# Kernel tuning notes

Hardware: AMD Instinct MI355X
Metric: run time of the kernel (lower is better)

The kernel has to match this reference:

```python
import jax, jax.numpy as jnp
import numpy as np

B, N, F_IN = 32, 1024, 128
H1, H2, OUT = 64, 32, 10
EDGE_P = 0.01  # edge probability for random adjacency


def setup_inputs() -> dict:
    key = jax.random.key(0)
    ks = jax.random.split(key, 16)
    x = jax.random.normal(ks[0], (B, N, F_IN), dtype=jnp.float32)
    # dense binary adjacency per graph (module consumes dense [N,N] adj)
    adj = (jax.random.uniform(ks[1], (B, N, N)) < EDGE_P).astype(jnp.float32)
    mask = jnp.ones((B, N, 1), dtype=jnp.float32)
    s = 0.05
    W1a = jax.random.normal(ks[2], (F_IN, H1), dtype=jnp.float32) * s
    b1a = jnp.zeros((H1,), dtype=jnp.float32)
    W2a = jax.random.normal(ks[3], (H1, H1), dtype=jnp.float32) * s
    b2a = jnp.zeros((H1,), dtype=jnp.float32)
    W1b = jax.random.normal(ks[4], (H1, H2), dtype=jnp.float32) * s
    b1b = jnp.zeros((H2,), dtype=jnp.float32)
    W2b = jax.random.normal(ks[5], (H2, H2), dtype=jnp.float32) * s
    b2b = jnp.zeros((H2,), dtype=jnp.float32)
    Wfc = jax.random.normal(ks[6], (H2, OUT), dtype=jnp.float32) * s
    bfc = jnp.zeros((OUT,), dtype=jnp.float32)
    return dict(x=x, adj=adj, mask=mask, W1a=W1a, b1a=b1a, W2a=W2a, b2a=b2a,
                W1b=W1b, b1b=b1b, W2b=W2b, b2b=b2b, Wfc=Wfc, bfc=bfc)


def _gin_layer(h, adj, mask, Wa, ba, Wb, bb, eps=0.0):
    # neighbor sum aggregation: neigh[b,i] = sum_j adj[b,i,j] * h[b,j]
    neigh = jnp.einsum('bij,bjf->bif', adj, h)
    z = (1.0 + eps) * h + neigh
    z = jax.nn.relu(z @ Wa + ba) @ Wb + bb  # 2-layer MLP
    return z * mask  # zero out padded nodes


def reference(x, adj, mask, W1a, b1a, W2a, b2a, W1b, b1b, W2b, b2b, Wfc, bfc):
    h = _gin_layer(x, adj, mask, W1a, b1a, W2a, b2a)   # [B,N,64]
    h = _gin_layer(h, adj, mask, W1b, b1b, W2b, b2b)   # [B,N,32]
    g = jnp.max(h, axis=1)                              # graph readout [B,32]
    return g @ Wfc + bfc                                # [B,OUT] (dropout = eval identity)
```

## Files before the change

### kernel.cpp

```cpp
#include <hip/hip_runtime.h>
#include <cstdint>
#include <cstddef>


#define CAP 64

typedef float v4f __attribute__((ext_vector_type(4)));

__device__ __forceinline__ float rl(float x, int l) {
  return __int_as_float(__builtin_amdgcn_readlane(__float_as_int(x), l));
}

__global__ __launch_bounds__(256) void k_scanproj(
    const float* __restrict__ x, const float* __restrict__ W1a,
    float* __restrict__ u,
    const float* __restrict__ adj, int* __restrict__ nbr,
    int* __restrict__ deg) {
  __shared__ float sW[128 * 64];
  int lane = threadIdx.x & 63;
  int wid  = threadIdx.x >> 6;
  if (blockIdx.x < 1024) {
    for (int t = threadIdx.x; t < 128 * 64; t += 256) sW[t] = W1a[t];
    __syncthreads();
    int row0 = (blockIdx.x * 4 + wid) * 8;
    row0 = __builtin_amdgcn_readfirstlane(row0);
    const float* xr = x + (size_t)row0 * 128;
    float acc[8] = {0, 0, 0, 0, 0, 0, 0, 0};
    for (int kc = 0; kc < 32; ++kc) {
      v4f xv[8];
      #pragma unroll
      for (int r = 0; r < 8; ++r)
        xv[r] = *(const v4f*)(xr + r * 128 + kc * 4);
      #pragma unroll
      for (int j = 0; j < 4; ++j) {
        float w = sW[(kc * 4 + j) * 64 + lane];
        #pragma unroll
        for (int r = 0; r < 8; ++r)
          acc[r] = fmaf(xv[r][j], w, acc[r]);
      }
    }
    #pragma unroll
    for (int r = 0; r < 8; ++r)
      u[(size_t)(row0 + r) * 64 + lane] = acc[r];
  } else {
    int node = (blockIdx.x - 1024) * 4 + wid;
    const v4f* arow = (const v4f*)(adj + (size_t)node * 1024);
    int* outp = nbr + node * CAP;
    v4f a[4];
    #pragma unroll
    for (int c = 0; c < 4; ++c)
      a[c] = __builtin_nontemporal_load(arow + c * 64 + lane);
    int cnt = 0;
    #pragma unroll
    for (int c = 0; c < 4; ++c) {
      #pragma unroll
      for (int comp = 0; comp < 4; ++comp) {
        bool hit = (a[c][comp] != 0.0f);
        unsigned long long m = __ballot(hit);
        if (hit) {
          int below = __builtin_amdgcn_mbcnt_hi(
              (unsigned)(m >> 32),
              __builtin_amdgcn_mbcnt_lo((unsigned)m, 0));
          int pos = cnt + below;
          if (pos < CAP) outp[pos] = ((c * 64 + lane) << 2) + comp;
        }
        cnt += __popcll(m);
      }
    }
    if (lane == 0) deg[node] = cnt < CAP ? cnt : CAP;
  }
}

__global__ __launch_bounds__(256) void k_gathA(
    const float* __restrict__ u, const int* __restrict__ nbr,
    const int* __restrict__ deg, const float* __restrict__ mask,
    const float* __restrict__ b1a, const float* __restrict__ W2a,
    const float* __restrict__ b2a, const float* __restrict__ W1b,
    float* __restrict__ v) {
  __shared__ float sW2[64 * 64];
  __shared__ float sW1b[64 * 32];
  for (int t = threadIdx.x; t < 64 * 64; t += 256) sW2[t] = W2a[t];
  for (int t = threadIdx.x; t < 64 * 32; t += 256) sW1b[t] = W1b[t];
  __syncthreads();
  int lane = threadIdx.x & 63;
  int f = lane & 31, hh = lane >> 5;
  float ba1 = b1a[lane], ba2 = b2a[lane];
  int gw = blockIdx.x * 4 + (threadIdx.x >> 6);
  int n0 = gw * 2, n1 = n0 + 1;
  const float* ub = u + (size_t)(n0 & ~1023) * 64;
  int d0 = deg[n0], d1 = deg[n1];
  int nl0 = nbr[n0 * CAP + lane], nl1 = nbr[n1 * CAP + lane];
  float s0[8] = {0,0,0,0,0,0,0,0}, s1[8] = {0,0,0,0,0,0,0,0};
  int dmax = d0 > d1 ? d0 : d1;
  int rounds = (dmax + 7) >> 3;
  for (int rr = 0; rr < rounds; ++rr) {
    int base = rr << 3;
    #pragma unroll
    for (int i = 0; i < 8; ++i) {
      int t = base + i;
      int j0 = __builtin_amdgcn_readlane(nl0, t);
      int j1 = __builtin_amdgcn_readlane(nl1, t);
      bool ok0 = t < d0, ok1 = t < d1;
      j0 = ok0 ? j0 : 0;  j1 = ok1 ? j1 : 0;
      float v0 = ub[j0 * 64 + lane];
      float v1 = ub[j1 * 64 + lane];
      s0[i] += ok0 ? v0 : 0.0f;
      s1[i] += ok1 ? v1 : 0.0f;
    }
  }
  float acc0 = ub[(n0 & 1023) * 64 + lane]
             + (((s0[0]+s0[1])+(s0[2]+s0[3]))+((s0[4]+s0[5])+(s0[6]+s0[7])));
  float acc1 = ub[(n1 & 1023) * 64 + lane]
             + (((s1[0]+s1[1])+(s1[2]+s1[3]))+((s1[4]+s1[5])+(s1[6]+s1[7])));
  float r0 = fmaxf(acc0 + ba1, 0.0f);
  float r1 = fmaxf(acc1 + ba1, 0.0f);
  float a0=0,a1=0,a2=0,a3=0, c0=0,c1=0,c2=0,c3=0;
  #pragma unroll
  for (int k = 0; k < 64; k += 4) {
    float w0 = sW2[(k    ) * 64 + lane];
    float w1 = sW2[(k + 1) * 64 + lane];
    float w2 = sW2[(k + 2) * 64 + lane];
    float w3 = sW2[(k + 3) * 64 + lane];
    a0 = fmaf(rl(r0, k    ), w0, a0);  c0 = fmaf(rl(r1, k    ), w0, c0);
    a1 = fmaf(rl(r0, k + 1), w1, a1);  c1 = fmaf(rl(r1, k + 1), w1, c1);
    a2 = fmaf(rl(r0, k + 2), w2, a2);  c2 = fmaf(rl(r1, k + 2), w2, c2);
    a3 = fmaf(rl(r0, k + 3), w3, a3);  c3 = fmaf(rl(r1, k + 3), w3, c3);
  }
  float h20 = (ba2 + ((a0 + a1) + (a2 + a3))) * mask[n0];
  float h21 = (ba2 + ((c0 + c1) + (c2 + c3))) * mask[n1];
  float p00=0,p01=0, p10=0,p11=0;
  #pragma unroll
  for (int k0 = 0; k0 < 32; k0 += 2) {
    float w0 = sW1b[(hh * 32 + k0    ) * 32 + f];
    float w1 = sW1b[(hh * 32 + k0 + 1) * 32 + f];
    p00 = fmaf(__shfl(h20, hh * 32 + k0    ), w0, p00);
    p01 = fmaf(__shfl(h20, hh * 32 + k0 + 1), w1, p01);
    p10 = fmaf(__shfl(h21, hh * 32 + k0    ), w0, p10);
    p11 = fmaf(__shfl(h21, hh * 32 + k0 + 1), w1, p11);
  }
  float vp0 = p00 + p01;  vp0 += __shfl_xor(vp0, 32);
  float vp1 = p10 + p11;  vp1 += __shfl_xor(vp1, 32);
  if (hh == 0) {
    v[n0 * 32 + f] = vp0;
    v[n1 * 32 + f] = vp1;
  }
}

__global__ __launch_bounds__(256) void k_gathB(
    const float* __restrict__ v, const int* __restrict__ nbr,
    const int* __restrict__ deg, const float* __restrict__ mask,
    const float* __restrict__ b1b, const float* __restrict__ W2b,
    const float* __restrict__ b2b, float* __restrict__ h3) {
  __shared__ float sW2b[32 * 32];
  for (int t = threadIdx.x; t < 32 * 32; t += 256) sW2b[t] = W2b[t];
  __syncthreads();
  int lane = threadIdx.x & 63;
  int f = lane & 31, hh = lane >> 5;
  float bb1 = b1b[f], bb2 = b2b[f];
  int gw = blockIdx.x * 4 + (threadIdx.x >> 6);
  int n0 = gw * 2, n1 = n0 + 1;
  const float* vb = v + (size_t)(n0 & ~1023) * 32;
  int d0 = deg[n0], d1 = deg[n1];
  int nl0 = nbr[n0 * CAP + lane], nl1 = nbr[n1 * CAP + lane];
  float s0[8] = {0,0,0,0,0,0,0,0}, s1[8] = {0,0,0,0,0,0,0,0};
  int dmax = d0 > d1 ? d0 : d1;
  int rounds = (dmax + 15) >> 4;
  for (int rr = 0; rr < rounds; ++rr) {
    int base = rr << 4;
    #pragma unroll
    for (int i = 0; i < 8; ++i) {
      int t = base + (i << 1) + hh;
      int j0 = __shfl(nl0, t);
      int j1 = __shfl(nl1, t);
      bool ok0 = t < d0, ok1 = t < d1;
      j0 = ok0 ? j0 : 0;  j1 = ok1 ? j1 : 0;
      float v0 = vb[j0 * 32 + f];
      float v1 = vb[j1 * 32 + f];
      s0[i] += ok0 ? v0 : 0.0f;
      s1[i] += ok1 ? v1 : 0.0f;
    }
  }
  float acc0 = ((s0[0]+s0[1])+(s0[2]+s0[3]))+((s0[4]+s0[5])+(s0[6]+s0[7]));
  float acc1 = ((s1[0]+s1[1])+(s1[2]+s1[3]))+((s1[4]+s1[5])+(s1[6]+s1[7]));
  acc0 += __shfl_xor(acc0, 32);
  acc1 += __shfl_xor(acc1, 32);
  float r0 = fmaxf(vb[(n0 & 1023) * 32 + f] + acc0 + bb1, 0.0f);
  float r1 = fmaxf(vb[(n1 & 1023) * 32 + f] + acc1 + bb1, 0.0f);
  float a0=0,a1=0,a2=0,a3=0, c0=0,c1=0,c2=0,c3=0;
  #pragma unroll
  for (int k = 0; k < 32; k += 4) {
    float w0 = sW2b[(k    ) * 32 + f];
    float w1 = sW2b[(k + 1) * 32 + f];
    float w2 = sW2b[(k + 2) * 32 + f];
    float w3 = sW2b[(k + 3) * 32 + f];
    a0 = fmaf(rl(r0, k    ), w0, a0);  c0 = fmaf(rl(r1, k    ), w0, c0);
    a1 = fmaf(rl(r0, k + 1), w1, a1);  c1 = fmaf(rl(r1, k + 1), w1, c1);
    a2 = fmaf(rl(r0, k + 2), w2, a2);  c2 = fmaf(rl(r1, k + 2), w2, c2);
    a3 = fmaf(rl(r0, k + 3), w3, a3);  c3 = fmaf(rl(r1, k + 3), w3, c3);
  }
  float o0 = (bb2 + ((a0 + a1) + (a2 + a3))) * mask[n0];
  float o1 = (bb2 + ((c0 + c1) + (c2 + c3))) * mask[n1];
  if (hh == 0) {
    h3[n0 * 32 + f] = o0;
    h3[n1 * 32 + f] = o1;
  }
}

__global__ __launch_bounds__(1024) void k_readout(
    const float* __restrict__ h3, const float* __restrict__ Wfc,
    const float* __restrict__ bfc, float* __restrict__ out) {
  __shared__ float red[32][33];
  __shared__ float g[32];
  int b = blockIdx.x;
  int f = threadIdx.x & 31, c = threadIdx.x >> 5;
  const float* hb = h3 + (size_t)b * 1024 * 32;
  float m = -3.4e38f;
  for (int r0 = 0; r0 < 32; ++r0)
    m = fmaxf(m, hb[(c * 32 + r0) * 32 + f]);
  red[c][f] = m;
  __syncthreads();
  if (c == 0) {
    float mm = red[0][f];
    #pragma unroll
    for (int k = 1; k < 32; ++k) mm = fmaxf(mm, red[k][f]);
    g[f] = mm;
  }
  __syncthreads();
  if (threadIdx.x < 10) {
    float o = bfc[threadIdx.x];
    #pragma unroll
    for (int k = 0; k < 32; ++k)
      o = fmaf(g[k], Wfc[k * 10 + threadIdx.x], o);
    out[b * 10 + threadIdx.x] = o;
  }
}

extern "C" void kernel_launch(void* const* d_in, const int* in_sizes, int n_in,
                              void* d_out, int out_size, void* d_ws, size_t ws_size,
                              hipStream_t stream) {
  const float* x    = (const float*)d_in[0];
  const float* adj  = (const float*)d_in[1];
  const float* mask = (const float*)d_in[2];
  const float* W1a  = (const float*)d_in[3];
  const float* b1a  = (const float*)d_in[4];
  const float* W2a  = (const float*)d_in[5];
  const float* b2a  = (const float*)d_in[6];
  const float* W1b  = (const float*)d_in[7];
  const float* b1b  = (const float*)d_in[8];
  const float* W2b  = (const float*)d_in[9];
  const float* b2b  = (const float*)d_in[10];
  const float* Wfc  = (const float*)d_in[11];
  const float* bfc  = (const float*)d_in[12];
  float* out = (float*)d_out;

  char* ws = (char*)d_ws;
  float* u   = (float*)(ws);
  float* v   = (float*)(ws + (8u << 20));
  int*   nbr = (int*)  (ws + (12u << 20));
  int*   deg = (int*)  (ws + (20u << 20));
  float* h3  = (float*)(ws);

  hipLaunchKernelGGL(k_scanproj, dim3(9216), dim3(256),  0, stream,
                     x, W1a, u, adj, nbr, deg);
  hipLaunchKernelGGL(k_gathA,    dim3(4096), dim3(256),  0, stream,
                     u, nbr, deg, mask, b1a, W2a, b2a, W1b, v);
  hipLaunchKernelGGL(k_gathB,    dim3(4096), dim3(256),  0, stream,
                     v, nbr, deg, mask, b1b, W2b, b2b, h3);
  hipLaunchKernelGGL(k_readout,  dim3(32),   dim3(1024), 0, stream,
                     h3, Wfc, bfc, out);
}
```

Measured before the change: 297.8 us.

## Remap gather blocks per XCD, fuse max readout into gathB, drop W1a LDS staging

The gather kernels now map block indices so that consecutive blocks on each XCD handle the same graph. This is meant to keep that graph's u/v rows in the XCD-local L2. gathB now reduces its per-block node max in LDS and writes a small partial-max buffer instead of the full h3 tensor, so the final readout kernel reads far less data. The projection kernel reads W1a straight from global/L1 instead of staging 32KB in LDS, which removes a barrier and LDS pressure but adds global loads inside the inner loop.

```diff
diff --git a/kernel.cpp b/kernel.cpp
--- a/kernel.cpp
+++ b/kernel.cpp
@@ -16,12 +16,9 @@
     float* __restrict__ u,
     const float* __restrict__ adj, int* __restrict__ nbr,
     int* __restrict__ deg) {
-  __shared__ float sW[128 * 64];
   int lane = threadIdx.x & 63;
   int wid  = threadIdx.x >> 6;
   if (blockIdx.x < 1024) {
-    for (int t = threadIdx.x; t < 128 * 64; t += 256) sW[t] = W1a[t];
-    __syncthreads();
     int row0 = (blockIdx.x * 4 + wid) * 8;
     row0 = __builtin_amdgcn_readfirstlane(row0);
     const float* xr = x + (size_t)row0 * 128;
@@ -33,7 +30,7 @@
         xv[r] = *(const v4f*)(xr + r * 128 + kc * 4);
       #pragma unroll
       for (int j = 0; j < 4; ++j) {
-        float w = sW[(kc * 4 + j) * 64 + lane];
+        float w = W1a[(kc * 4 + j) * 64 + lane];
         #pragma unroll
         for (int r = 0; r < 8; ++r)
           acc[r] = fmaf(xv[r][j], w, acc[r]);
@@ -85,9 +82,12 @@
   int lane = threadIdx.x & 63;
   int f = lane & 31, hh = lane >> 5;
   float ba1 = b1a[lane], ba2 = b2a[lane];
-  int gw = blockIdx.x * 4 + (threadIdx.x >> 6);
-  int n0 = gw * 2, n1 = n0 + 1;
-  const float* ub = u + (size_t)(n0 & ~1023) * 64;
+  int i = blockIdx.x, wid = threadIdx.x >> 6;
+  int xcd = i & 7, j = i >> 3;
+  int b = xcd + 8 * (j & 3);
+  int w = j >> 2;
+  int n0 = b * 1024 + w * 8 + wid * 2, n1 = n0 + 1;
+  const float* ub = u + (size_t)b * 1024 * 64;
   int d0 = deg[n0], d1 = deg[n1];
   int nl0 = nbr[n0 * CAP + lane], nl1 = nbr[n1 * CAP + lane];
   float s0[8] = {0,0,0,0,0,0,0,0}, s1[8] = {0,0,0,0,0,0,0,0};
@@ -96,16 +96,16 @@
   for (int rr = 0; rr < rounds; ++rr) {
     int base = rr << 3;
     #pragma unroll
-    for (int i = 0; i < 8; ++i) {
-      int t = base + i;
+    for (int i2 = 0; i2 < 8; ++i2) {
+      int t = base + i2;
       int j0 = __builtin_amdgcn_readlane(nl0, t);
       int j1 = __builtin_amdgcn_readlane(nl1, t);
       bool ok0 = t < d0, ok1 = t < d1;
       j0 = ok0 ? j0 : 0;  j1 = ok1 ? j1 : 0;
       float v0 = ub[j0 * 64 + lane];
       float v1 = ub[j1 * 64 + lane];
-      s0[i] += ok0 ? v0 : 0.0f;
-      s1[i] += ok1 ? v1 : 0.0f;
+      s0[i2] += ok0 ? v0 : 0.0f;
+      s1[i2] += ok1 ? v1 : 0.0f;
     }
   }
   float acc0 = ub[(n0 & 1023) * 64 + lane]
@@ -150,16 +150,20 @@
     const float* __restrict__ v, const int* __restrict__ nbr,
     const int* __restrict__ deg, const float* __restrict__ mask,
     const float* __restrict__ b1b, const float* __restrict__ W2b,
-    const float* __restrict__ b2b, float* __restrict__ h3) {
+    const float* __restrict__ b2b, float* __restrict__ pmax) {
   __shared__ float sW2b[32 * 32];
+  __shared__ float wred[4][32];
   for (int t = threadIdx.x; t < 32 * 32; t += 256) sW2b[t] = W2b[t];
   __syncthreads();
   int lane = threadIdx.x & 63;
   int f = lane & 31, hh = lane >> 5;
   float bb1 = b1b[f], bb2 = b2b[f];
-  int gw = blockIdx.x * 4 + (threadIdx.x >> 6);
-  int n0 = gw * 2, n1 = n0 + 1;
-  const float* vb = v + (size_t)(n0 & ~1023) * 32;
+  int i = blockIdx.x, wid = threadIdx.x >> 6;
+  int xcd = i & 7, j = i >> 3;
+  int b = xcd + 8 * (j & 3);
+  int w = j >> 2;
+  int n0 = b * 1024 + w * 8 + wid * 2, n1 = n0 + 1;
+  const float* vb = v + (size_t)b * 1024 * 32;
   int d0 = deg[n0], d1 = deg[n1];
   int nl0 = nbr[n0 * CAP + lane], nl1 = nbr[n1 * CAP + lane];
   float s0[8] = {0,0,0,0,0,0,0,0}, s1[8] = {0,0,0,0,0,0,0,0};
@@ -168,16 +172,16 @@
   for (int rr = 0; rr < rounds; ++rr) {
     int base = rr << 4;
     #pragma unroll
-    for (int i = 0; i < 8; ++i) {
-      int t = base + (i << 1) + hh;
+    for (int i2 = 0; i2 < 8; ++i2) {
+      int t = base + (i2 << 1) + hh;
       int j0 = __shfl(nl0, t);
       int j1 = __shfl(nl1, t);
       bool ok0 = t < d0, ok1 = t < d1;
       j0 = ok0 ? j0 : 0;  j1 = ok1 ? j1 : 0;
       float v0 = vb[j0 * 32 + f];
       float v1 = vb[j1 * 32 + f];
-      s0[i] += ok0 ? v0 : 0.0f;
-      s1[i] += ok1 ? v1 : 0.0f;
+      s0[i2] += ok0 ? v0 : 0.0f;
+      s1[i2] += ok1 ? v1 : 0.0f;
     }
   }
   float acc0 = ((s0[0]+s0[1])+(s0[2]+s0[3]))+((s0[4]+s0[5])+(s0[6]+s0[7]));
@@ -200,23 +204,28 @@
   }
   float o0 = (bb2 + ((a0 + a1) + (a2 + a3))) * mask[n0];
   float o1 = (bb2 + ((c0 + c1) + (c2 + c3))) * mask[n1];
-  if (hh == 0) {
-    h3[n0 * 32 + f] = o0;
-    h3[n1 * 32 + f] = o1;
-  }
-}
-
-__global__ __launch_bounds__(1024) void k_readout(
-    const float* __restrict__ h3, const float* __restrict__ Wfc,
+  float m = fmaxf(o0, o1);
+  if (hh == 0) wred[wid][f] = m;
+  __syncthreads();
+  if (threadIdx.x < 32) {
+    float mm = fmaxf(fmaxf(wred[0][threadIdx.x], wred[1][threadIdx.x]),
+                     fmaxf(wred[2][threadIdx.x], wred[3][threadIdx.x]));
+    pmax[((b << 7) + w) * 32 + threadIdx.x] = mm;
+  }
+}
+
+__global__ __launch_bounds__(1024) void k_fin(
+    const float* __restrict__ pmax, const float* __restrict__ Wfc,
     const float* __restrict__ bfc, float* __restrict__ out) {
   __shared__ float red[32][33];
   __shared__ float g[32];
   int b = blockIdx.x;
   int f = threadIdx.x & 31, c = threadIdx.x >> 5;
-  const float* hb = h3 + (size_t)b * 1024 * 32;
+  const float* pb = pmax + (size_t)b * 128 * 32;
   float m = -3.4e38f;
-  for (int r0 = 0; r0 < 32; ++r0)
-    m = fmaxf(m, hb[(c * 32 + r0) * 32 + f]);
+  #pragma unroll
+  for (int q = 0; q < 4; ++q)
+    m = fmaxf(m, pb[(c * 4 + q) * 32 + f]);
   red[c][f] = m;
   __syncthreads();
   if (c == 0) {
@@ -254,18 +263,18 @@
   float* out = (float*)d_out;
 
   char* ws = (char*)d_ws;
-  float* u   = (float*)(ws);
-  float* v   = (float*)(ws + (8u << 20));
-  int*   nbr = (int*)  (ws + (12u << 20));
-  int*   deg = (int*)  (ws + (20u << 20));
-  float* h3  = (float*)(ws);
+  float* u    = (float*)(ws);
+  float* v    = (float*)(ws + (8u << 20));
+  int*   nbr  = (int*)  (ws + (12u << 20));
+  int*   deg  = (int*)  (ws + (20u << 20));
+  float* pmax = (float*)(ws + (21u << 20));
 
   hipLaunchKernelGGL(k_scanproj, dim3(9216), dim3(256),  0, stream,
                      x, W1a, u, adj, nbr, deg);
   hipLaunchKernelGGL(k_gathA,    dim3(4096), dim3(256),  0, stream,
                      u, nbr, deg, mask, b1a, W2a, b2a, W1b, v);
   hipLaunchKernelGGL(k_gathB,    dim3(4096), dim3(256),  0, stream,
-                     v, nbr, deg, mask, b1b, W2b, b2b, h3);
-  hipLaunchKernelGGL(k_readout,  dim3(32),   dim3(1024), 0, stream,
-                     h3, Wfc, bfc, out);
-}
+                     v, nbr, deg, mask, b1b, W2b, b2b, pmax);
+  hipLaunchKernelGGL(k_fin,      dim3(32),   dim3(1024), 0, stream,
+                     pmax, Wfc, bfc, out);
+}
```

New measurement: 274.0 us. 8.0% less time.
